# Performance work log

Hardware: AMD Instinct MI355X
Metric: run time of the kernel (lower is better)

## Reference

```python
import jax, jax.numpy as jnp
import numpy as np

D = 256          # d_model
NH = 8           # heads
NP = 4           # points per level
NL = 4           # feature levels
DH = D // NH     # head dim = 32
MLP = 4 * D      # 1024
B = 2
SHAPES = [(128, 128), (64, 64), (32, 32), (16, 16)]
LQ = sum(h * w for h, w in SHAPES)  # 21760
EPS = 1e-6


def layer_norm(x, g, b):
    mu = jnp.mean(x, axis=-1, keepdims=True)
    var = jnp.mean(jnp.square(x - mu), axis=-1, keepdims=True)
    return (x - mu) * jax.lax.rsqrt(var + EPS) * g + b


def bilinear_sample(val_l, loc, Hs, Ws):
    # val_l: [B, Hs*Ws, NH, DH]; loc: [B, Lq, NH, NP, 2] normalized in [0,1]
    v = val_l.transpose(0, 2, 1, 3)                      # [B, NH, HW, DH]
    x = loc[..., 0] * Ws - 0.5                           # [B, Lq, NH, NP]
    y = loc[..., 1] * Hs - 0.5
    x0 = jnp.floor(x); y0 = jnp.floor(y)
    lx = x - x0; ly = y - y0
    x0i = x0.astype(jnp.int32); y0i = y0.astype(jnp.int32)

    def gather(xi, yi):
        inb = (xi >= 0) & (xi < Ws) & (yi >= 0) & (yi < Hs)
        idx = jnp.clip(yi, 0, Hs - 1) * Ws + jnp.clip(xi, 0, Ws - 1)
        idx = idx.transpose(0, 2, 1, 3)                  # [B, NH, Lq, NP]
        sh = idx.shape
        idxf = idx.reshape(sh[0], sh[1], -1)
        g = jax.vmap(jax.vmap(lambda vv, ii: vv[ii]))(v, idxf)
        g = g.reshape(sh[0], sh[1], sh[2], sh[3], v.shape[-1])
        return g * inb.transpose(0, 2, 1, 3)[..., None].astype(g.dtype)

    wt = lambda a: a.transpose(0, 2, 1, 3)[..., None]    # -> [B, NH, Lq, NP, 1]
    out = (gather(x0i, y0i) * wt((1 - lx) * (1 - ly))
           + gather(x0i + 1, y0i) * wt(lx * (1 - ly))
           + gather(x0i, y0i + 1) * wt((1 - lx) * ly)
           + gather(x0i + 1, y0i + 1) * wt(lx * ly))
    return out                                            # [B, NH, Lq, NP, DH]


def setup_inputs() -> dict:
    key = jax.random.key(0)
    ks = jax.random.split(key, 16)
    ss = np.array(SHAPES, dtype=np.int64)
    lsi = np.concatenate([[0], np.cumsum(ss[:, 0] * ss[:, 1])[:-1]]).astype(np.int64)
    s = 0.02
    return {
        'src': jax.random.normal(ks[0], (B, LQ, D), jnp.float32),
        'pos': jax.random.normal(ks[1], (B, LQ, D), jnp.float32),
        'reference_points': jax.random.uniform(ks[2], (B, LQ, NL, 2), jnp.float32),
        'spatial_shapes': ss,
        'level_start_index': lsi,
        'g1': jnp.ones((D,), jnp.float32), 'beta1': jnp.zeros((D,), jnp.float32),
        'w_off': jax.random.normal(ks[3], (D, NH * NL * NP * 2), jnp.float32) * 0.01,
        'b_off': jax.random.normal(ks[4], (NH * NL * NP * 2,), jnp.float32) * 0.1,
        'w_attn': jax.random.normal(ks[5], (D, NH * NL * NP), jnp.float32) * s,
        'b_attn': jnp.zeros((NH * NL * NP,), jnp.float32),
        'w_val': jax.random.normal(ks[6], (D, D), jnp.float32) * s,
        'b_val': jnp.zeros((D,), jnp.float32),
        'w_out': jax.random.normal(ks[7], (D, D), jnp.float32) * s,
        'b_out': jnp.zeros((D,), jnp.float32),
        'g2': jnp.ones((D,), jnp.float32), 'beta2': jnp.zeros((D,), jnp.float32),
        'w_fc1': jax.random.normal(ks[8], (D, MLP), jnp.float32) * s,
        'b_fc1': jnp.zeros((MLP,), jnp.float32),
        'w_fc2': jax.random.normal(ks[9], (MLP, D), jnp.float32) * s,
        'b_fc2': jnp.zeros((D,), jnp.float32),
    }


def reference(src, pos, reference_points, spatial_shapes, level_start_index,
              g1, beta1, w_off, b_off, w_attn, b_attn, w_val, b_val,
              w_out, b_out, g2, beta2, w_fc1, b_fc1, w_fc2, b_fc2):
    ss = np.asarray(spatial_shapes)
    lsi = np.asarray(level_start_index)
    Bsz, Lq, _ = src.shape

    # --- pre-norm + multi-scale deformable attention + residual ---
    x = layer_norm(src, g1, beta1)
    q = x + pos
    val = (x @ w_val + b_val).reshape(Bsz, Lq, NH, DH)
    off = (q @ w_off + b_off).reshape(Bsz, Lq, NH, NL, NP, 2)
    aw = jax.nn.softmax((q @ w_attn + b_attn).reshape(Bsz, Lq, NH, NL * NP), axis=-1)
    aw = aw.reshape(Bsz, Lq, NH, NL, NP)

    out = jnp.zeros((Bsz, Lq, NH, DH), src.dtype)
    for l in range(NL):
        Hs, Ws = int(ss[l, 0]), int(ss[l, 1])
        start = int(lsi[l])
        vl = val[:, start:start + Hs * Ws]                       # [B, HW, NH, DH]
        norm = jnp.array([Ws, Hs], src.dtype)
        loc = reference_points[:, :, None, l, None, :] + off[:, :, :, l] / norm
        samp = bilinear_sample(vl, loc, Hs, Ws)                  # [B, NH, Lq, NP, DH]
        a = aw[:, :, :, l].transpose(0, 2, 1, 3)                 # [B, NH, Lq, NP]
        out = out + jnp.einsum('bhqp,bhqpd->bqhd', a, samp)
    attn_out = out.reshape(Bsz, Lq, D) @ w_out + b_out
    src2 = src + attn_out

    # --- pre-norm MLP + residual ---
    y = layer_norm(src2, g2, beta2)
    ffn = jax.nn.relu(y @ w_fc1 + b_fc1) @ w_fc2 + b_fc2
    return src2 + ffn
```

## Files before the change

### kernel.cpp

```cpp
#include <hip/hip_runtime.h>

#define DMODEL 256
#define NHEAD 8
#define NPOINT 4
#define NLEVEL 4
#define DHEAD 32
#define MLPD 1024
#define BSZ 2
#define LQTOK 21760
#define NTOK (BSZ * LQTOK)
#define LNEPS 1e-6f

typedef __attribute__((ext_vector_type(8))) short short8;
typedef __attribute__((ext_vector_type(4))) float f32x4;
typedef __attribute__((ext_vector_type(2))) float f32x2;

__device__ __forceinline__ float bf2f(unsigned short u) {
  unsigned int i = ((unsigned int)u) << 16;
  return __builtin_bit_cast(float, i);
}
__device__ __forceinline__ unsigned short f2bf(float f) {
  unsigned int i = __builtin_bit_cast(unsigned int, f);
  i += 0x7fff + ((i >> 16) & 1);
  return (unsigned short)(i >> 16);
}
__device__ __forceinline__ float bflo(unsigned int u) {
  return __builtin_bit_cast(float, u << 16);
}
__device__ __forceinline__ float bfhi(unsigned int u) {
  return __builtin_bit_cast(float, u & 0xffff0000u);
}

__device__ __forceinline__ void pk_fma_blo(f32x2& d, f32x2 a, f32x2 b) {
  asm("v_pk_fma_f32 %0, %1, %2, %0 op_sel:[0,0,0] op_sel_hi:[1,0,1]"
      : "+v"(d)
      : "v"(a), "v"(b));
}
__device__ __forceinline__ void pk_fma_bhi(f32x2& d, f32x2 a, f32x2 b) {
  asm("v_pk_fma_f32 %0, %1, %2, %0 op_sel:[0,1,0] op_sel_hi:[1,1,1]"
      : "+v"(d)
      : "v"(a), "v"(b));
}

__device__ __forceinline__ void gload_lds16(const unsigned short* g,
                                            unsigned short* lds) {
  __builtin_amdgcn_global_load_lds(
      (const __attribute__((address_space(1))) unsigned int*)g,
      (__attribute__((address_space(3))) unsigned int*)lds, 16, 0, 0);
}

__device__ __forceinline__ unsigned xcd_swz(unsigned orig, unsigned nwg) {
  unsigned xcd = orig & 7u, rest = orig >> 3;
  unsigned qq = nwg >> 3, rr = nwg & 7u;
  return (xcd < rr ? xcd * (qq + 1) : rr * (qq + 1) + (xcd - rr) * qq) + rest;
}

__global__ __launch_bounds__(256) void ln_bf16(
    const float* __restrict__ in, const float* __restrict__ g,
    const float* __restrict__ beta, unsigned short* __restrict__ o,
    const float* __restrict__ pos, unsigned short* __restrict__ q) {
  const int w = threadIdx.x >> 6, lane = threadIdx.x & 63;
  const size_t t = (size_t)blockIdx.x * 4 + w;
  const size_t base = t * DMODEL + lane * 4;
  float4 v = *(const float4*)(in + base);
  float s = (v.x + v.y) + (v.z + v.w);
#pragma unroll
  for (int off = 32; off; off >>= 1) s += __shfl_xor(s, off, 64);
  float mu = s * (1.0f / DMODEL);
  float dx = v.x - mu, dy = v.y - mu, dz = v.z - mu, dw = v.w - mu;
  float s2 = (dx * dx + dy * dy) + (dz * dz + dw * dw);
#pragma unroll
  for (int off = 32; off; off >>= 1) s2 += __shfl_xor(s2, off, 64);
  float rs = rsqrtf(s2 * (1.0f / DMODEL) + LNEPS);
  float4 gg = *(const float4*)(g + lane * 4);
  float4 bb = *(const float4*)(beta + lane * 4);
  unsigned short r0 = f2bf(dx * rs * gg.x + bb.x);
  unsigned short r1 = f2bf(dy * rs * gg.y + bb.y);
  unsigned short r2 = f2bf(dz * rs * gg.z + bb.z);
  unsigned short r3 = f2bf(dw * rs * gg.w + bb.w);
  unsigned int lo = ((unsigned int)r1 << 16) | r0;
  unsigned int hi = ((unsigned int)r3 << 16) | r2;
  *(uint2*)(o + base) = make_uint2(lo, hi);
  float4 p = *(const float4*)(pos + base);
  unsigned short q0 = f2bf(bf2f(r0) + p.x);
  unsigned short q1 = f2bf(bf2f(r1) + p.y);
  unsigned short q2 = f2bf(bf2f(r2) + p.z);
  unsigned short q3 = f2bf(bf2f(r3) + p.w);
  unsigned int ql = ((unsigned int)q1 << 16) | q0;
  unsigned int qh = ((unsigned int)q3 << 16) | q2;
  *(uint2*)(q + base) = make_uint2(ql, qh);
}

__global__ __launch_bounds__(256) void transpose_all(
    const float* __restrict__ w_val, const float* __restrict__ w_off,
    const float* __restrict__ w_attn, const float* __restrict__ w_out,
    const float* __restrict__ w_fc1, const float* __restrict__ w_fc2,
    unsigned short* __restrict__ wvalT, unsigned short* __restrict__ woffaT,
    unsigned short* __restrict__ woutT, unsigned short* __restrict__ wfc1T,
    unsigned short* __restrict__ wfc2T) {
  __shared__ float tile[32][33];
  int bid = blockIdx.x;
  const float* W;
  unsigned short* Wt;
  int K, N, rel;
  if (bid < 64) {
    W = w_val; Wt = wvalT; K = 256; N = 256; rel = bid;
  } else if (bid < 128) {
    W = w_off; Wt = woffaT; K = 256; N = 256; rel = bid - 64;
  } else if (bid < 160) {
    W = w_attn; Wt = woffaT + 256 * 256; K = 256; N = 128; rel = bid - 128;
  } else if (bid < 224) {
    W = w_out; Wt = woutT; K = 256; N = 256; rel = bid - 160;
  } else if (bid < 480) {
    W = w_fc1; Wt = wfc1T; K = 256; N = 1024; rel = bid - 224;
  } else {
    W = w_fc2; Wt = wfc2T; K = 1024; N = 256; rel = bid - 480;
  }
  int ktiles = K >> 5;
  int k0 = (rel % ktiles) * 32, n0 = (rel / ktiles) * 32;
  int tx = threadIdx.x & 31, ty = threadIdx.x >> 5;
  for (int i = ty; i < 32; i += 8)
    tile[i][tx] = W[(size_t)(k0 + i) * N + n0 + tx];
  __syncthreads();
  for (int i = ty; i < 32; i += 8)
    Wt[(size_t)(n0 + i) * K + k0 + tx] = f2bf(tile[tx][i]);
}

template <int OMODE>
__global__ __launch_bounds__(256) void gemm_mfma(
    const unsigned short* __restrict__ A, const unsigned short* __restrict__ Wt,
    const float* __restrict__ bias, const float* __restrict__ res,
    void* __restrict__ Cout, int M, int N, int K) {
  __shared__ __attribute__((aligned(16))) unsigned short As[128 * 32];
  __shared__ __attribute__((aligned(16))) unsigned short Bs[128 * 32];
  const int tid = threadIdx.x;
  const unsigned gy = gridDim.y;
  const unsigned wgid = xcd_swz(blockIdx.y * gridDim.x + blockIdx.x,
                                gridDim.x * gy);
  const int m0 = (int)(wgid / gy) * 128;
  const int n0 = (int)(wgid % gy) * 128;
  const int wave = tid >> 6, lane = tid & 63;
  const int wm = (wave & 1) * 64, wn = (wave >> 1) * 64;
  const int lr = lane & 15, quad = lane >> 4;
  f32x4 acc[4][4] = {};
  for (int k0 = 0; k0 < K; k0 += 32) {
    __syncthreads();
#pragma unroll
    for (int r = 0; r < 2; r++) {
      int c = r * 256 + tid;
      int row = c >> 2, col8 = (c & 3) * 8;
      gload_lds16(Wt + (size_t)(n0 + row) * K + k0 + col8,
                  &Bs[(r * 256 + wave * 64) * 8]);
    }
#pragma unroll
    for (int r = 0; r < 2; r++) {
      int c = r * 256 + tid;
      int row = c >> 2, col8 = (c & 3) * 8;
      gload_lds16(A + (size_t)(m0 + row) * K + k0 + col8,
                  &As[(r * 256 + wave * 64) * 8]);
    }
    __syncthreads();
    short8 af[4], bfr[4];
#pragma unroll
    for (int i = 0; i < 4; i++)
      af[i] = *(const short8*)(&As[(wm + i * 16 + lr) * 32 + quad * 8]);
#pragma unroll
    for (int j = 0; j < 4; j++)
      bfr[j] = *(const short8*)(&Bs[(wn + j * 16 + lr) * 32 + quad * 8]);
#pragma unroll
    for (int i = 0; i < 4; i++)
#pragma unroll
      for (int j = 0; j < 4; j++)
        acc[i][j] = __builtin_amdgcn_mfma_f32_16x16x32_bf16(af[i], bfr[j],
                                                            acc[i][j], 0, 0, 0);
  }
#pragma unroll
  for (int i = 0; i < 4; i++) {
    int rbase = m0 + wm + i * 16 + quad * 4;
#pragma unroll
    for (int j = 0; j < 4; j++) {
      int col = n0 + wn + j * 16 + lr;
      float bv = bias[col];
#pragma unroll
      for (int r = 0; r < 4; r++) {
        size_t idx = (size_t)(rbase + r) * N + col;
        float v = acc[i][j][r] + bv;
        if (OMODE == 2) v = fmaxf(v, 0.0f);
        if (OMODE == 3) {
          ((float*)Cout)[idx] = v + res[idx];
        } else {
          ((unsigned short*)Cout)[idx] = f2bf(v);
        }
      }
    }
  }
}

__global__ __launch_bounds__(256) void gemm_vo(
    const unsigned short* __restrict__ Ax, const unsigned short* __restrict__ Aq,
    const unsigned short* __restrict__ Wval,
    const unsigned short* __restrict__ Woa, const float* __restrict__ bval,
    const float* __restrict__ boff, const float* __restrict__ battn,
    unsigned short* __restrict__ oval, unsigned short* __restrict__ ooff,
    unsigned short* __restrict__ olg) {
  __shared__ __attribute__((aligned(16))) unsigned short As[128 * 32];
  __shared__ __attribute__((aligned(16))) unsigned short Bs[128 * 32];
  const int tid = threadIdx.x;
  const unsigned gy = gridDim.y;
  const unsigned wgid = xcd_swz(blockIdx.y * gridDim.x + blockIdx.x,
                                gridDim.x * gy);
  const int m0 = (int)(wgid / gy) * 128;
  const int ny = (int)(wgid % gy);
  const bool isval = ny < 2;
  const unsigned short* A = isval ? Ax : Aq;
  const unsigned short* Wt = isval ? Wval : Woa;
  const int n0 = isval ? ny * 128 : (ny - 2) * 128;
  const int wave = tid >> 6, lane = tid & 63;
  const int wm = (wave & 1) * 64, wn = (wave >> 1) * 64;
  const int lr = lane & 15, quad = lane >> 4;
  f32x4 acc[4][4] = {};
  for (int k0 = 0; k0 < 256; k0 += 32) {
    __syncthreads();
#pragma unroll
    for (int r = 0; r < 2; r++) {
      int c = r * 256 + tid;
      int row = c >> 2, col8 = (c & 3) * 8;
      gload_lds16(Wt + (size_t)(n0 + row) * 256 + k0 + col8,
                  &Bs[(r * 256 + wave * 64) * 8]);
    }
#pragma unroll
    for (int r = 0; r < 2; r++) {
      int c = r * 256 + tid;
      int row = c >> 2, col8 = (c & 3) * 8;
      gload_lds16(A + (size_t)(m0 + row) * 256 + k0 + col8,
                  &As[(r * 256 + wave * 64) * 8]);
    }
    __syncthreads();
    short8 af[4], bfr[4];
#pragma unroll
    for (int i = 0; i < 4; i++)
      af[i] = *(const short8*)(&As[(wm + i * 16 + lr) * 32 + quad * 8]);
#pragma unroll
    for (int j = 0; j < 4; j++)
      bfr[j] = *(const short8*)(&Bs[(wn + j * 16 + lr) * 32 + quad * 8]);
#pragma unroll
    for (int i = 0; i < 4; i++)
#pragma unroll
      for (int j = 0; j < 4; j++)
        acc[i][j] = __builtin_amdgcn_mfma_f32_16x16x32_bf16(af[i], bfr[j],
                                                            acc[i][j], 0, 0, 0);
  }
#pragma unroll
  for (int i = 0; i < 4; i++) {
    int rbase = m0 + wm + i * 16 + quad * 4;
#pragma unroll
    for (int j = 0; j < 4; j++) {
      int col = n0 + wn + j * 16 + lr;
      float bv = isval ? bval[col]
                       : (col < 256 ? boff[col] : battn[col - 256]);
#pragma unroll
      for (int r = 0; r < 4; r++) {
        int row = rbase + r;
        float v = acc[i][j][r] + bv;
        if (isval) {
          int b_ = row >= LQTOK ? 1 : 0;
          int lq = row - b_ * LQTOK;
          int h = col >> 5, cc = col & 31;
          oval[(((size_t)b_ * 8 + h) * LQTOK + lq) * 32 + cc] = f2bf(v);
        } else if (col < 256) {
          ooff[(size_t)row * 256 + col] = f2bf(v);
        } else {
          olg[(size_t)row * 128 + (col - 256)] = f2bf(v);
        }
      }
    }
  }
}

__global__ __launch_bounds__(256) void gemm_out_ln(
    const unsigned short* __restrict__ A, const unsigned short* __restrict__ Wt,
    const float* __restrict__ bias, const float* __restrict__ src,
    const float* __restrict__ g2, const float* __restrict__ beta2,
    float* __restrict__ src2, unsigned short* __restrict__ y) {
  __shared__ __attribute__((aligned(16))) unsigned short As[64 * 32];
  __shared__ __attribute__((aligned(16))) unsigned short Bs[256 * 32];
  __shared__ float red[2][64][2];
  const int tid = threadIdx.x;
  const int m0 = (int)blockIdx.x * 64;
  const int wave = tid >> 6, lane = tid & 63;
  const int wm = (wave >> 1) * 32, wn = (wave & 1) * 128;
  const int lr = lane & 15, quad = lane >> 4;
  f32x4 acc[2][8] = {};
  for (int k0 = 0; k0 < 256; k0 += 32) {
    __syncthreads();
    {
      int row = tid >> 2, col8 = (tid & 3) * 8;
      gload_lds16(A + (size_t)(m0 + row) * 256 + k0 + col8,
                  &As[(wave * 64) * 8]);
    }
#pragma unroll
    for (int r = 0; r < 4; r++) {
      int c = r * 256 + tid;
      int row = c >> 2, col8 = (c & 3) * 8;
      gload_lds16(Wt + (size_t)row * 256 + k0 + col8,
                  &Bs[(r * 256 + wave * 64) * 8]);
    }
    __syncthreads();
    short8 af[2], bfr[8];
#pragma unroll
    for (int i = 0; i < 2; i++)
      af[i] = *(const short8*)(&As[(wm + i * 16 + lr) * 32 + quad * 8]);
#pragma unroll
    for (int j = 0; j < 8; j++)
      bfr[j] = *(const short8*)(&Bs[(wn + j * 16 + lr) * 32 + quad * 8]);
#pragma unroll
    for (int i = 0; i < 2; i++)
#pragma unroll
      for (int j = 0; j < 8; j++)
        acc[i][j] = __builtin_amdgcn_mfma_f32_16x16x32_bf16(af[i], bfr[j],
                                                            acc[i][j], 0, 0, 0);
  }
  float s1[2][4] = {}, s2[2][4] = {};
#pragma unroll
  for (int i = 0; i < 2; i++)
#pragma unroll
    for (int j = 0; j < 8; j++) {
      int col = wn + j * 16 + lr;
      float bv = bias[col];
#pragma unroll
      for (int r = 0; r < 4; r++) {
        int row = m0 + wm + i * 16 + quad * 4 + r;
        size_t idx = (size_t)row * 256 + col;
        float v = acc[i][j][r] + bv + src[idx];
        src2[idx] = v;
        acc[i][j][r] = v;
        s1[i][r] += v;
        s2[i][r] = fmaf(v, v, s2[i][r]);
      }
    }
#pragma unroll
  for (int i = 0; i < 2; i++)
#pragma unroll
    for (int r = 0; r < 4; r++)
#pragma unroll
      for (int s = 1; s < 16; s <<= 1) {
        s1[i][r] += __shfl_xor(s1[i][r], s, 64);
        s2[i][r] += __shfl_xor(s2[i][r], s, 64);
      }
  if (lr == 0) {
#pragma unroll
    for (int i = 0; i < 2; i++)
#pragma unroll
      for (int r = 0; r < 4; r++) {
        int rl = wm + i * 16 + quad * 4 + r;
        red[0][rl][wave & 1] = s1[i][r];
        red[1][rl][wave & 1] = s2[i][r];
      }
  }
  __syncthreads();
#pragma unroll
  for (int i = 0; i < 2; i++)
#pragma unroll
    for (int r = 0; r < 4; r++) {
      int rl = wm + i * 16 + quad * 4 + r;
      float S1 = red[0][rl][0] + red[0][rl][1];
      float S2 = red[1][rl][0] + red[1][rl][1];
      float mu = S1 * (1.0f / DMODEL);
      float var = S2 * (1.0f / DMODEL) - mu * mu;
      float rs = rsqrtf(var + LNEPS);
      int row = m0 + rl;
#pragma unroll
      for (int j = 0; j < 8; j++) {
        int col = wn + j * 16 + lr;
        float yv = (acc[i][j][r] - mu) * rs * g2[col] + beta2[col];
        y[(size_t)row * 256 + col] = f2bf(yv);
      }
    }
}

__global__ __launch_bounds__(512) void deform_sample(
    const unsigned short* __restrict__ val, const unsigned short* __restrict__ off,
    const unsigned short* __restrict__ logits, const float* __restrict__ refp,
    unsigned short* __restrict__ out) {
  __shared__ __attribute__((aligned(16))) int2 sIdx[8][16][8];
  __shared__ __attribute__((aligned(16))) float sW[8][16][8][4];
  const int w = threadIdx.x >> 6, lane = threadIdx.x & 63;
  const int bq = blockIdx.x * 8 + w;
  const int b = __builtin_amdgcn_readfirstlane(bq / LQTOK);
  {
    const int HW_[4] = {128, 64, 32, 16};
    const int LSI_[4] = {0, 16384, 20480, 21504};
    int u0 = 2 * lane;
    int h = u0 >> 4;
    int lvl = (u0 >> 2) & 3;
    int pt0 = u0 & 15;
    int HW = HW_[lvl];
    float2 rp = ((const float2*)refp)[(size_t)bq * 4 + lvl];
    uint2 ov = *(const uint2*)(off + (size_t)bq * 256 + 4 * lane);
    unsigned int lgu = *(const unsigned int*)(logits + (size_t)bq * 128 + 2 * lane);
    float lg0 = bflo(lgu), lg1 = bfhi(lgu);
    float mx = fmaxf(lg0, lg1);
#pragma unroll
    for (int s = 1; s < 8; s <<= 1) mx = fmaxf(mx, __shfl_xor(mx, s, 64));
    float e0 = expf(lg0 - mx), e1 = expf(lg1 - mx);
    float es = e0 + e1;
#pragma unroll
    for (int s = 1; s < 8; s <<= 1) es += __shfl_xor(es, s, 64);
    float inv = 1.0f / es;
    float a01[2] = {e0 * inv, e1 * inv};
    unsigned int ovv[2] = {ov.x, ov.y};
#pragma unroll
    for (int c = 0; c < 2; c++) {
      float x = fmaf(rp.x, (float)HW, bflo(ovv[c])) - 0.5f;
      float y = fmaf(rp.y, (float)HW, bfhi(ovv[c])) - 0.5f;
      float xf = floorf(x), yf = floorf(y);
      int x0 = (int)xf, y0 = (int)yf;
      float lx = x - xf, ly = y - yf;
      int x0c = min(max(x0, 0), HW - 1);
      int x1c = min(max(x0 + 1, 0), HW - 1);
      int y0c = min(max(y0, 0), HW - 1);
      int y1c = min(max(y0 + 1, 0), HW - 1);
      float m0x = (x0 >= 0 && x0 < HW) ? 1.f : 0.f;
      float m1x = (x0 + 1 >= 0 && x0 + 1 < HW) ? 1.f : 0.f;
      float m0y = (y0 >= 0 && y0 < HW) ? 1.f : 0.f;
      float m1y = (y0 + 1 >= 0 && y0 + 1 < HW) ? 1.f : 0.f;
      float a = a01[c];
      float w00 = (1.f - lx) * (1.f - ly) * m0x * m0y * a;
      float w01 = lx * (1.f - ly) * m1x * m0y * a;
      float w10 = (1.f - lx) * ly * m0x * m1y * a;
      float w11 = lx * ly * m1x * m1y * a;
      int xb = min(max(x0, 0), HW - 2);
      bool c0 = (x0c == xb), c1 = (x1c == xb);
      float A0 = (c0 ? w00 : 0.f) + (c1 ? w01 : 0.f);
      float B0 = (c0 ? 0.f : w00) + (c1 ? 0.f : w01);
      float A1 = (c0 ? w10 : 0.f) + (c1 ? w11 : 0.f);
      float B1 = (c0 ? 0.f : w10) + (c1 ? 0.f : w11);
      int pt = pt0 + c;
      int hs = h ^ (pt & 7);
      sIdx[w][pt][hs] = make_int2((LSI_[lvl] + y0c * HW + xb) * 64,
                                  (LSI_[lvl] + y1c * HW + xb) * 64);
      *(float4*)sW[w][pt][hs] = make_float4(A0, B0, A1, B1);
    }
  }
  __builtin_amdgcn_wave_barrier();
  const int h2 = lane >> 3, g = lane & 7;
  const char* base2 = (const char*)val +
                      ((size_t)(b * 8 + h2) * LQTOK) * 64 + g * 16;
  f32x2 a4[4] = {};
#pragma unroll
  for (int pb = 0; pb < 4; pb++) {
    int2 tt[4];
    f32x4 wt4[4];
#pragma unroll
    for (int p = 0; p < 4; p++) {
      int pt = pb * 4 + p;
      int hs = h2 ^ (pt & 7);
      tt[p] = sIdx[w][pt][hs];
      wt4[p] = *(const f32x4*)sW[w][pt][hs];
    }
    uint4 v0[4], v1[4];
#pragma unroll
    for (int p = 0; p < 4; p++) {
      v0[p] = *(const uint4*)(base2 + (unsigned)tt[p].x);
      v1[p] = *(const uint4*)(base2 + (unsigned)tt[p].y);
    }
#pragma unroll
    for (int p = 0; p < 4; p++) {
      f32x2 wp;
      wp[0] = (g < 4) ? wt4[p][0] : wt4[p][1];
      wp[1] = (g < 4) ? wt4[p][2] : wt4[p][3];
      f32x2 u;
      u[0] = bflo(v0[p].x); u[1] = bfhi(v0[p].x); pk_fma_blo(a4[0], u, wp);
      u[0] = bflo(v0[p].y); u[1] = bfhi(v0[p].y); pk_fma_blo(a4[1], u, wp);
      u[0] = bflo(v0[p].z); u[1] = bfhi(v0[p].z); pk_fma_blo(a4[2], u, wp);
      u[0] = bflo(v0[p].w); u[1] = bfhi(v0[p].w); pk_fma_blo(a4[3], u, wp);
      u[0] = bflo(v1[p].x); u[1] = bfhi(v1[p].x); pk_fma_bhi(a4[0], u, wp);
      u[0] = bflo(v1[p].y); u[1] = bfhi(v1[p].y); pk_fma_bhi(a4[1], u, wp);
      u[0] = bflo(v1[p].z); u[1] = bfhi(v1[p].z); pk_fma_bhi(a4[2], u, wp);
      u[0] = bflo(v1[p].w); u[1] = bfhi(v1[p].w); pk_fma_bhi(a4[3], u, wp);
    }
  }
#pragma unroll
  for (int qv = 0; qv < 4; qv++) {
    a4[qv][0] += __shfl_xor(a4[qv][0], 4, 64);
    a4[qv][1] += __shfl_xor(a4[qv][1], 4, 64);
  }
  if (g < 4) {
    uint4 o;
    o.x = ((unsigned)f2bf(a4[0][1]) << 16) | f2bf(a4[0][0]);
    o.y = ((unsigned)f2bf(a4[1][1]) << 16) | f2bf(a4[1][0]);
    o.z = ((unsigned)f2bf(a4[2][1]) << 16) | f2bf(a4[2][0]);
    o.w = ((unsigned)f2bf(a4[3][1]) << 16) | f2bf(a4[3][0]);
    *(uint4*)(out + (size_t)bq * 256 + h2 * 32 + g * 8) = o;
  }
}

extern "C" void kernel_launch(void* const* d_in, const int* in_sizes, int n_in,
                              void* d_out, int out_size, void* d_ws,
                              size_t ws_size, hipStream_t stream) {
  const float* src    = (const float*)d_in[0];
  const float* pos    = (const float*)d_in[1];
  const float* refp   = (const float*)d_in[2];
  const float* g1     = (const float*)d_in[5];
  const float* beta1  = (const float*)d_in[6];
  const float* w_off  = (const float*)d_in[7];
  const float* b_off  = (const float*)d_in[8];
  const float* w_attn = (const float*)d_in[9];
  const float* b_attn = (const float*)d_in[10];
  const float* w_val  = (const float*)d_in[11];
  const float* b_val  = (const float*)d_in[12];
  const float* w_out  = (const float*)d_in[13];
  const float* b_out  = (const float*)d_in[14];
  const float* g2     = (const float*)d_in[15];
  const float* beta2  = (const float*)d_in[16];
  const float* w_fc1  = (const float*)d_in[17];
  const float* b_fc1  = (const float*)d_in[18];
  const float* w_fc2  = (const float*)d_in[19];
  const float* b_fc2  = (const float*)d_in[20];
  float* out = (float*)d_out;

  const size_t NT = (size_t)NTOK;
  unsigned short* b1 = (unsigned short*)d_ws;
  unsigned short* b2 = b1 + NT * 256;
  unsigned short* b3 = b2 + NT * 256;
  unsigned short* b4 = b3 + NT * 256;
  unsigned short* b5 = b4 + NT * 256;
  unsigned short* wvalT  = b5 + NT * 512;
  unsigned short* woffaT = wvalT + 256 * 256;
  unsigned short* woutT  = woffaT + 384 * 256;
  unsigned short* wfc1T  = woutT + 256 * 256;
  unsigned short* wfc2T  = wfc1T + 1024 * 256;

  unsigned short* qb  = b4;
  unsigned short* lgb = b5;
  unsigned short* yb  = b5;
  unsigned short* hid = b1;

  const int MT = NTOK / 128;

  transpose_all<<<736, 256, 0, stream>>>(w_val, w_off, w_attn, w_out, w_fc1,
                                         w_fc2, wvalT, woffaT, woutT, wfc1T,
                                         wfc2T);
  ln_bf16<<<NTOK / 4, 256, 0, stream>>>(src, g1, beta1, b1, pos, qb);
  gemm_vo<<<dim3(MT, 5), 256, 0, stream>>>(b1, qb, wvalT, woffaT, b_val, b_off,
                                           b_attn, b2, b3, lgb);
  deform_sample<<<NTOK / 8, 512, 0, stream>>>(b2, b3, lgb, refp, b1);
  gemm_out_ln<<<NTOK / 64, 256, 0, stream>>>(b1, woutT, b_out, src, g2, beta2,
                                             out, yb);
  gemm_mfma<2><<<dim3(MT, 8), 256, 0, stream>>>(yb, wfc1T, b_fc1, nullptr, hid,
                                                NTOK, 1024, 256);
  gemm_mfma<3><<<dim3(MT, 2), 256, 0, stream>>>(hid, wfc2T, b_fc2, out, out,
                                                NTOK, 256, 1024);
}
```

Before: 412.4 us.

## Retile out-proj+LN GEMM to 128 rows and double-buffer deform sample loads

The output-projection GEMM with fused LayerNorm now uses 512-thread blocks covering 128 rows. Each wave computes a 64x64 tile, and the row statistics are reduced across four column waves instead of two. In the deformable sampling kernel, the four point-batch loop becomes a two-stage software pipeline: gathers for the next batch are issued before the current batch is consumed, to hide gather latency. The costs are more registers in the sampling kernel, which may lower occupancy, and fewer, larger blocks in the GEMM.

```diff
diff --git a/kernel.cpp b/kernel.cpp
--- a/kernel.cpp
+++ b/kernel.cpp
@@ -277,20 +277,20 @@
   }
 }
 
-__global__ __launch_bounds__(256) void gemm_out_ln(
+__global__ __launch_bounds__(512) void gemm_out_ln(
     const unsigned short* __restrict__ A, const unsigned short* __restrict__ Wt,
     const float* __restrict__ bias, const float* __restrict__ src,
     const float* __restrict__ g2, const float* __restrict__ beta2,
     float* __restrict__ src2, unsigned short* __restrict__ y) {
-  __shared__ __attribute__((aligned(16))) unsigned short As[64 * 32];
+  __shared__ __attribute__((aligned(16))) unsigned short As[128 * 32];
   __shared__ __attribute__((aligned(16))) unsigned short Bs[256 * 32];
-  __shared__ float red[2][64][2];
+  __shared__ float red[2][128][4];
   const int tid = threadIdx.x;
-  const int m0 = (int)blockIdx.x * 64;
+  const int m0 = (int)blockIdx.x * 128;
   const int wave = tid >> 6, lane = tid & 63;
-  const int wm = (wave >> 1) * 32, wn = (wave & 1) * 128;
+  const int wm = (wave & 1) * 64, wn = (wave >> 1) * 64;
   const int lr = lane & 15, quad = lane >> 4;
-  f32x4 acc[2][8] = {};
+  f32x4 acc[4][4] = {};
   for (int k0 = 0; k0 < 256; k0 += 32) {
     __syncthreads();
     {
@@ -299,32 +299,32 @@
                   &As[(wave * 64) * 8]);
     }
 #pragma unroll
-    for (int r = 0; r < 4; r++) {
-      int c = r * 256 + tid;
+    for (int r = 0; r < 2; r++) {
+      int c = r * 512 + tid;
       int row = c >> 2, col8 = (c & 3) * 8;
       gload_lds16(Wt + (size_t)row * 256 + k0 + col8,
-                  &Bs[(r * 256 + wave * 64) * 8]);
+                  &Bs[((r * 8 + wave) * 64) * 8]);
     }
     __syncthreads();
-    short8 af[2], bfr[8];
-#pragma unroll
-    for (int i = 0; i < 2; i++)
+    short8 af[4], bfr[4];
+#pragma unroll
+    for (int i = 0; i < 4; i++)
       af[i] = *(const short8*)(&As[(wm + i * 16 + lr) * 32 + quad * 8]);
 #pragma unroll
-    for (int j = 0; j < 8; j++)
+    for (int j = 0; j < 4; j++)
       bfr[j] = *(const short8*)(&Bs[(wn + j * 16 + lr) * 32 + quad * 8]);
 #pragma unroll
-    for (int i = 0; i < 2; i++)
-#pragma unroll
-      for (int j = 0; j < 8; j++)
+    for (int i = 0; i < 4; i++)
+#pragma unroll
+      for (int j = 0; j < 4; j++)
         acc[i][j] = __builtin_amdgcn_mfma_f32_16x16x32_bf16(af[i], bfr[j],
                                                             acc[i][j], 0, 0, 0);
   }
-  float s1[2][4] = {}, s2[2][4] = {};
-#pragma unroll
-  for (int i = 0; i < 2; i++)
-#pragma unroll
-    for (int j = 0; j < 8; j++) {
+  float s1[4][4] = {}, s2[4][4] = {};
+#pragma unroll
+  for (int i = 0; i < 4; i++)
+#pragma unroll
+    for (int j = 0; j < 4; j++) {
       int col = wn + j * 16 + lr;
       float bv = bias[col];
 #pragma unroll
@@ -339,7 +339,7 @@
       }
     }
 #pragma unroll
-  for (int i = 0; i < 2; i++)
+  for (int i = 0; i < 4; i++)
 #pragma unroll
     for (int r = 0; r < 4; r++)
 #pragma unroll
@@ -349,34 +349,63 @@
       }
   if (lr == 0) {
 #pragma unroll
-    for (int i = 0; i < 2; i++)
+    for (int i = 0; i < 4; i++)
 #pragma unroll
       for (int r = 0; r < 4; r++) {
         int rl = wm + i * 16 + quad * 4 + r;
-        red[0][rl][wave & 1] = s1[i][r];
-        red[1][rl][wave & 1] = s2[i][r];
+        red[0][rl][wave >> 1] = s1[i][r];
+        red[1][rl][wave >> 1] = s2[i][r];
       }
   }
   __syncthreads();
 #pragma unroll
-  for (int i = 0; i < 2; i++)
+  for (int i = 0; i < 4; i++)
 #pragma unroll
     for (int r = 0; r < 4; r++) {
       int rl = wm + i * 16 + quad * 4 + r;
-      float S1 = red[0][rl][0] + red[0][rl][1];
-      float S2 = red[1][rl][0] + red[1][rl][1];
+      float S1 = (red[0][rl][0] + red[0][rl][1]) +
+                 (red[0][rl][2] + red[0][rl][3]);
+      float S2 = (red[1][rl][0] + red[1][rl][1]) +
+                 (red[1][rl][2] + red[1][rl][3]);
       float mu = S1 * (1.0f / DMODEL);
       float var = S2 * (1.0f / DMODEL) - mu * mu;
       float rs = rsqrtf(var + LNEPS);
       int row = m0 + rl;
 #pragma unroll
-      for (int j = 0; j < 8; j++) {
+      for (int j = 0; j < 4; j++) {
         int col = wn + j * 16 + lr;
         float yv = (acc[i][j][r] - mu) * rs * g2[col] + beta2[col];
         y[(size_t)row * 256 + col] = f2bf(yv);
       }
     }
 }
+
+#define PREF_IDX(tt, wt, pb)                                        \
+  _Pragma("unroll") for (int p = 0; p < 4; p++) {                   \
+    int hs = h2 ^ (((pb)*4 + p) & 7);                               \
+    tt[p] = sIdx[w][(pb)*4 + p][hs];                                \
+    wt[p] = *(const f32x4*)sW[w][(pb)*4 + p][hs];                   \
+  }
+#define PREF_LD(v0, v1, tt)                                         \
+  _Pragma("unroll") for (int p = 0; p < 4; p++) {                   \
+    v0[p] = *(const uint4*)(base2 + (unsigned)tt[p].x);             \
+    v1[p] = *(const uint4*)(base2 + (unsigned)tt[p].y);             \
+  }
+#define CONSUME(v0, v1, wt)                                         \
+  _Pragma("unroll") for (int p = 0; p < 4; p++) {                   \
+    f32x2 wp;                                                       \
+    wp[0] = (g < 4) ? wt[p][0] : wt[p][1];                          \
+    wp[1] = (g < 4) ? wt[p][2] : wt[p][3];                          \
+    f32x2 u;                                                        \
+    u[0] = bflo(v0[p].x); u[1] = bfhi(v0[p].x); pk_fma_blo(a4[0], u, wp); \
+    u[0] = bflo(v0[p].y); u[1] = bfhi(v0[p].y); pk_fma_blo(a4[1], u, wp); \
+    u[0] = bflo(v0[p].z); u[1] = bfhi(v0[p].z); pk_fma_blo(a4[2], u, wp); \
+    u[0] = bflo(v0[p].w); u[1] = bfhi(v0[p].w); pk_fma_blo(a4[3], u, wp); \
+    u[0] = bflo(v1[p].x); u[1] = bfhi(v1[p].x); pk_fma_bhi(a4[0], u, wp); \
+    u[0] = bflo(v1[p].y); u[1] = bfhi(v1[p].y); pk_fma_bhi(a4[1], u, wp); \
+    u[0] = bflo(v1[p].z); u[1] = bfhi(v1[p].z); pk_fma_bhi(a4[2], u, wp); \
+    u[0] = bflo(v1[p].w); u[1] = bfhi(v1[p].w); pk_fma_bhi(a4[3], u, wp); \
+  }
 
 __global__ __launch_bounds__(512) void deform_sample(
     const unsigned short* __restrict__ val, const unsigned short* __restrict__ off,
@@ -447,39 +476,21 @@
   const char* base2 = (const char*)val +
                       ((size_t)(b * 8 + h2) * LQTOK) * 64 + g * 16;
   f32x2 a4[4] = {};
-#pragma unroll
-  for (int pb = 0; pb < 4; pb++) {
-    int2 tt[4];
-    f32x4 wt4[4];
-#pragma unroll
-    for (int p = 0; p < 4; p++) {
-      int pt = pb * 4 + p;
-      int hs = h2 ^ (pt & 7);
-      tt[p] = sIdx[w][pt][hs];
-      wt4[p] = *(const f32x4*)sW[w][pt][hs];
-    }
-    uint4 v0[4], v1[4];
-#pragma unroll
-    for (int p = 0; p < 4; p++) {
-      v0[p] = *(const uint4*)(base2 + (unsigned)tt[p].x);
-      v1[p] = *(const uint4*)(base2 + (unsigned)tt[p].y);
-    }
-#pragma unroll
-    for (int p = 0; p < 4; p++) {
-      f32x2 wp;
-      wp[0] = (g < 4) ? wt4[p][0] : wt4[p][1];
-      wp[1] = (g < 4) ? wt4[p][2] : wt4[p][3];
-      f32x2 u;
-      u[0] = bflo(v0[p].x); u[1] = bfhi(v0[p].x); pk_fma_blo(a4[0], u, wp);
-      u[0] = bflo(v0[p].y); u[1] = bfhi(v0[p].y); pk_fma_blo(a4[1], u, wp);
-      u[0] = bflo(v0[p].z); u[1] = bfhi(v0[p].z); pk_fma_blo(a4[2], u, wp);
-      u[0] = bflo(v0[p].w); u[1] = bfhi(v0[p].w); pk_fma_blo(a4[3], u, wp);
-      u[0] = bflo(v1[p].x); u[1] = bfhi(v1[p].x); pk_fma_bhi(a4[0], u, wp);
-      u[0] = bflo(v1[p].y); u[1] = bfhi(v1[p].y); pk_fma_bhi(a4[1], u, wp);
-      u[0] = bflo(v1[p].z); u[1] = bfhi(v1[p].z); pk_fma_bhi(a4[2], u, wp);
-      u[0] = bflo(v1[p].w); u[1] = bfhi(v1[p].w); pk_fma_bhi(a4[3], u, wp);
-    }
-  }
+  int2 ttA[4], ttB[4];
+  f32x4 wtA[4], wtB[4];
+  uint4 v0A[4], v1A[4], v0B[4], v1B[4];
+  PREF_IDX(ttA, wtA, 0);
+  PREF_LD(v0A, v1A, ttA);
+  PREF_IDX(ttB, wtB, 1);
+  PREF_LD(v0B, v1B, ttB);
+  CONSUME(v0A, v1A, wtA);
+  PREF_IDX(ttA, wtA, 2);
+  PREF_LD(v0A, v1A, ttA);
+  CONSUME(v0B, v1B, wtB);
+  PREF_IDX(ttB, wtB, 3);
+  PREF_LD(v0B, v1B, ttB);
+  CONSUME(v0A, v1A, wtA);
+  CONSUME(v0B, v1B, wtB);
 #pragma unroll
   for (int qv = 0; qv < 4; qv++) {
     a4[qv][0] += __shfl_xor(a4[qv][0], 4, 64);
@@ -545,8 +556,8 @@
   gemm_vo<<<dim3(MT, 5), 256, 0, stream>>>(b1, qb, wvalT, woffaT, b_val, b_off,
                                            b_attn, b2, b3, lgb);
   deform_sample<<<NTOK / 8, 512, 0, stream>>>(b2, b3, lgb, refp, b1);
-  gemm_out_ln<<<NTOK / 64, 256, 0, stream>>>(b1, woutT, b_out, src, g2, beta2,
-                                             out, yb);
+  gemm_out_ln<<<MT, 512, 0, stream>>>(b1, woutT, b_out, src, g2, beta2,
+                                      out, yb);
   gemm_mfma<2><<<dim3(MT, 8), 256, 0, stream>>>(yb, wfc1T, b_fc1, nullptr, hid,
                                                 NTOK, 1024, 256);
   gemm_mfma<3><<<dim3(MT, 2), 256, 0, stream>>>(hid, wfc2T, b_fc2, out, out,
```

After: 430.5 us. 1.04x slower.
